# Optimization experiments

Hardware: AMD Instinct MI355X
Metric: run time of the kernel (lower is better)

## Reference

```python
import jax, jax.numpy as jnp
import numpy as np
import math

B_GRAPHS = 256
L_NODES = 64
N_NODES = B_GRAPHS * L_NODES
N_EDGES = N_NODES * 4
HEADS = 8
D_INNER = 512
N_DAGS = 1
DIAMETER = 64


def setup_inputs() -> dict:
    key = jax.random.key(0)
    ks = jax.random.split(key, 8)
    x = jax.random.normal(ks[0], (N_NODES, D_INNER), jnp.float32)
    B = jax.random.normal(ks[1], (N_NODES, D_INNER), jnp.float32)
    C = jax.random.normal(ks[2], (N_NODES, D_INNER), jnp.float32)
    dt = jax.random.normal(ks[3], (N_NODES, N_DAGS * HEADS * 2), jnp.float32)
    dt_edge = jax.random.normal(ks[4], (N_EDGES, N_DAGS * HEADS), jnp.float32)
    # DAG edges: within each graph, src_local < dst_local (gap 1..7) -> strictly upper triangular
    u = jax.random.randint(ks[5], (N_EDGES,), 0, L_NODES - 1)
    gap = jax.random.randint(ks[6], (N_EDGES,), 1, 8)
    v = jnp.minimum(u + gap, L_NODES - 1)
    graph = jnp.arange(N_EDGES) // (N_EDGES // B_GRAPHS)
    edge_index = jnp.stack([graph * L_NODES + u, graph * L_NODES + v]).astype(jnp.int32)
    data_batch = (jnp.arange(N_NODES) // L_NODES).astype(jnp.int32)
    dag_masks = jnp.ones((N_DAGS, N_EDGES), jnp.float32)
    # dt_bias init as in module __init__ (inverse softplus of dt in [1e-3, 1e-1])
    rng = np.random.default_rng(0)
    dtv = np.exp(rng.uniform(size=(HEADS,)) * (math.log(0.1) - math.log(0.001)) + math.log(0.001))
    dtv = np.clip(dtv, 1e-4, None)
    dt_bias = jnp.asarray(dtv + np.log(-np.expm1(-dtv)), jnp.float32)
    D = jnp.ones((HEADS,), jnp.float32)
    return dict(x=x, B=B, C=C, dt=dt, dt_edge=dt_edge, dt_bias=dt_bias, D=D,
                dag_masks=dag_masks, edge_index=edge_index, data_batch=data_batch,
                diameter=DIAMETER)


def _repeated_squaring_inverse(A, diam):
    # (I - A)^{-1} = prod_k (I + A^{2^k}) for nilpotent A; O(log diam) matmuls
    j = 2 ** int(math.ceil(math.log2(diam)))
    I = jnp.eye(A.shape[-1], dtype=A.dtype)
    last = A
    M = I + A
    for _ in range(2, int(math.log2(j)) + 1):
        last = last @ last
        M = M @ (I + last)
    return M


def reference(x, B, C, dt, dt_edge, dt_bias, D, dag_masks, edge_index, data_batch, diameter):
    N, din = x.shape
    g, E = dag_masks.shape
    n = dt_bias.shape[0]
    b = int(data_batch[-1]) + 1
    l = N // b  # equal-size graphs -> dense batching is a reshape, mask all-True
    h = din // n
    src, dst = edge_index[0], edge_index[1]

    # dt_node: (N, g*n*c) -> (c, g, n, N); softplus(dt + bias)
    c = dt.shape[1] // (g * n)
    dtn = dt.reshape(N, g, n, c).transpose(3, 1, 2, 0)
    dtn = jax.nn.softplus(dtn + dt_bias[None, None, :, None])
    dte = dt_edge.reshape(E, g, n).transpose(1, 2, 0)  # (g,n,E)
    dte = jax.nn.softplus(dte + dt_bias[None, :, None])

    dt_s, dt_t = dtn[0], dtn[1]
    dt_sum = (dt_s[:, :, src] + dt_t[:, :, dst] + dte) / np.sqrt(3.0)  # (g,n,E)
    dt_exp = jnp.exp(-dt_sum)
    msk = dag_masks[:, None, :]
    dt_sum = dt_sum * msk
    dt_exp = dt_exp * msk

    # dense adjacency with per-edge attrs; note 'b l1 l2 (g n) -> b g n l2 l1' transpose
    b_e = src // l
    sl = src % l
    dl = dst % l
    attr = dt_exp.transpose(2, 0, 1).reshape(E, g * n)
    adj = jnp.zeros((b, l, l, g * n), x.dtype).at[b_e, sl, dl].add(attr)
    A = adj.reshape(b, l, l, g, n).transpose(0, 3, 4, 2, 1)  # (b,g,n,l,l)

    # normalize_mat: sqrt outer product of in-degree counts, clamped at 1
    ec = jnp.zeros((g, N), x.dtype).at[:, dst].add(dag_masks)
    ec_dense = ec.T.reshape(b, l, g)
    outer = jnp.sqrt(jnp.einsum('blg,btg->bglt', ec_dense, ec_dense))
    outer = jnp.where(outer < 1.0, 1.0, outer)
    A = A / outer[:, :, None]

    dnorm = jnp.zeros((g, n, N), x.dtype).at[:, :, dst].add(dt_sum)
    dnorm = dnorm.transpose(2, 0, 1).reshape(b, l, g, n).transpose(0, 2, 3, 1)  # (b,g,n,l)

    A2 = A.reshape(b, g * n, l, l).astype(jnp.float32)
    L = _repeated_squaring_inverse(A2, int(diameter))
    L = L.reshape(b, g, n, l, l) * dnorm[..., None]

    x4 = x.reshape(b, l, n, h).transpose(0, 2, 1, 3)  # (b,n,l,h)
    B3 = B.reshape(b, l, -1)
    C3 = C.reshape(b, l, -1)
    # y = einsum(C,L,B,x) with B/C broadcast over (g,n): fold C.B^T into L
    CB = jnp.einsum('bld,btd->blt', C3, B3)
    M = L * CB[:, None, None]
    y = jnp.einsum('bgnlt,bnth->bgnlh', M, x4)
    y = y + x4[:, None] * D[None, None, :, None, None]
    y = y.transpose(0, 3, 1, 2, 4).reshape(N, g, n * h)  # b g n l h -> (N, g, n*h)
    y = y.sum(axis=1) / np.sqrt(g)
    return y
```

## Files before the change

### kernel.cpp

```cpp
#include <hip/hip_runtime.h>
#include <math.h>

#define NGRAPH 256
#define HEADS  8
#define DIN    512
#define EPG    256
#define NEDGE  65536
#define LOG2E 1.44269504088896341f
#define LN2   0.69314718055994531f

typedef short bf16x8 __attribute__((ext_vector_type(8)));
typedef float f32x4 __attribute__((ext_vector_type(4)));
typedef unsigned long long u64;

__device__ __forceinline__ float softplusf(float v) {
    if (v > 20.f) return v;
    float t = exp2f(v * LOG2E);
    return LN2 * log2f(1.f + t);
}
__device__ __forceinline__ unsigned short f2bf(float f) {
    union { float f; unsigned u; } c; c.f = f;
    unsigned r = c.u + 0x7fffu + ((c.u >> 16) & 1u);
    return (unsigned short)(r >> 16);
}
__device__ __forceinline__ float bf2f(unsigned short h) {
    union { float f; unsigned u; } c; c.u = ((unsigned)h) << 16;
    return c.f;
}
__device__ __forceinline__ int swz_idx(int row, int t) {
    int g = ((t >> 3) ^ (row ^ (row >> 3))) & 7;
    return (row << 6) | (g << 3) | (t & 7);
}
__device__ __forceinline__ void split1(float f, unsigned short& hi, unsigned short& lo) {
    union { float f; unsigned q; } c; c.f = f;
    unsigned hb = c.q & 0xffff0000u;
    hi = (unsigned short)(hb >> 16);
    union { float f; unsigned q; } d; d.q = hb;
    union { float f; unsigned q; } e2; e2.f = f - d.f;
    lo = (unsigned short)(e2.q >> 16);
}

__global__ __launch_bounds__(512, 2) void dag_pipe_v6(
        const float* __restrict__ x,
        const float* __restrict__ Bm,
        const float* __restrict__ Cm,
        const float* __restrict__ dt,
        const float* __restrict__ dt_edge,
        const float* __restrict__ dt_bias,
        const float* __restrict__ Dp,
        const float* __restrict__ dag_masks,
        const int* __restrict__ edge_index,
        float* __restrict__ out) {
    __shared__ __align__(16) unsigned short WS[32768];
    __shared__ __align__(16) unsigned short Xt[HEADS][4096];
    __shared__ __align__(16) unsigned short CBsh[4096];
    __shared__ __align__(16) float Ab8[HEADS][512];
    __shared__ float dts[HEADS][64];
    __shared__ float dtt[HEADS][64];
    __shared__ float ecsh[HEADS][64];

    const int b = blockIdx.x;
    const int tid = threadIdx.x;
    const int w = tid >> 6;
    const int lane = tid & 63;
    const int lm = lane & 15;
    const int quad = lane >> 4;
    const float bias = dt_bias[w];

    float2 dv = *(const float2*)(dt + ((size_t)(b * 64 + lane)) * 16 + w * 2);

    const int u0 = tid * 4;
    const int mat = u0 >> 10;
    const int srow = (u0 & 1023) >> 4;
    const int scol = (u0 & 15) << 2;
    const float* sp = (mat ? Bm : Cm) + ((size_t)(b * 64 + srow)) * DIN + scol;

    float4 pre0[4], pre1[4];
    #pragma unroll
    for (int i = 0; i < 4; ++i) pre0[i] = *(const float4*)(sp + 0 * 64 + 4 * i);
    #pragma unroll
    for (int i = 0; i < 4; ++i) pre1[i] = *(const float4*)(sp + 1 * 64 + 4 * i);

    int esl[4], edl[4]; float emk[4], edr[4];
    #pragma unroll
    for (int eo = 0; eo < 4; ++eo) {
        int e = b * EPG + eo * 64 + lane;
        esl[eo] = edge_index[e];
        edl[eo] = edge_index[NEDGE + e];
        emk[eo] = dag_masks[e];
        edr[eo] = dt_edge[(size_t)e * HEADS + w];
    }

    float4 xv[16];
    const float* xg = x + (size_t)b * 64 * DIN + w * 64;
    #pragma unroll
    for (int r = 0; r < 4; ++r) {
        int t0 = quad * 4 + r * 16;
        #pragma unroll
        for (int k = 0; k < 4; ++k)
            xv[r * 4 + k] = *(const float4*)(xg + (size_t)(t0 + k) * DIN + lm * 4);
    }

    dts[w][lane] = softplusf(dv.x + bias);
    dtt[w][lane] = softplusf(dv.y + bias);
    ecsh[w][lane] = 0.f;
    {
        float4 z = make_float4(0.f, 0.f, 0.f, 0.f);
        *(float4*)(&Ab8[w][lane * 8]) = z;
        *(float4*)(&Ab8[w][lane * 8 + 4]) = z;
    }

    #pragma unroll
    for (int eo = 0; eo < 4; ++eo) {
        int sl = esl[eo] & 63;
        int dl = edl[eo] & 63;
        float de = softplusf(edr[eo] + bias);
        float dsum = (dts[w][sl] + dtt[w][dl] + de) * 0.57735026918962576451f;
        float dexp = exp2f(-dsum * LOG2E);
        atomicAdd(&Ab8[w][dl * 8 + (dl - sl)], dexp * emk[eo]);
        atomicAdd(&Ab8[w][dl * 8], dsum * emk[eo]);
        atomicAdd(&ecsh[w][dl], emk[eo]);
    }

    const int mi = w >> 1;
    const int ni0 = (w & 1) * 2;
    f32x4 acc0 = {0.f, 0.f, 0.f, 0.f};
    f32x4 acc1 = {0.f, 0.f, 0.f, 0.f};
    #pragma unroll
    for (int c = 0; c < 8; ++c) {
        unsigned short* buf = WS + (c & 1) * 16384;
        unsigned short* thi = buf + mat * 8192;
        #pragma unroll
        for (int i = 0; i < 4; ++i) {
            float4 v = (c & 1) ? pre1[i] : pre0[i];
            float a[4] = {v.x, v.y, v.z, v.w};
            u64 hp = 0, lp = 0;
            #pragma unroll
            for (int k = 0; k < 4; ++k) {
                unsigned short h, l;
                split1(a[k], h, l);
                hp |= ((u64)h) << (16 * k);
                lp |= ((u64)l) << (16 * k);
            }
            int idx = swz_idx(srow, scol + 4 * i);
            *(u64*)(thi + idx) = hp;
            *(u64*)(thi + 4096 + idx) = lp;
        }
        if (c + 2 < 8) {
            #pragma unroll
            for (int i = 0; i < 4; ++i) {
                float4 nv = *(const float4*)(sp + (c + 2) * 64 + 4 * i);
                if (c & 1) pre1[i] = nv; else pre0[i] = nv;
            }
        }
        __syncthreads();
        const unsigned short* p = buf;
        #pragma unroll
        for (int ks = 0; ks < 2; ++ks) {
            int kl = ks * 32 + quad * 8;
            bf16x8 ah  = *(const bf16x8*)(p +         swz_idx(mi * 16 + lm, kl));
            bf16x8 al  = *(const bf16x8*)(p +  4096 + swz_idx(mi * 16 + lm, kl));
            bf16x8 b0h = *(const bf16x8*)(p +  8192 + swz_idx(ni0 * 16 + lm, kl));
            bf16x8 b0l = *(const bf16x8*)(p + 12288 + swz_idx(ni0 * 16 + lm, kl));
            bf16x8 b1h = *(const bf16x8*)(p +  8192 + swz_idx((ni0 + 1) * 16 + lm, kl));
            bf16x8 b1l = *(const bf16x8*)(p + 12288 + swz_idx((ni0 + 1) * 16 + lm, kl));
            acc0 = __builtin_amdgcn_mfma_f32_16x16x32_bf16(ah, b0h, acc0, 0, 0, 0);
            acc0 = __builtin_amdgcn_mfma_f32_16x16x32_bf16(ah, b0l, acc0, 0, 0, 0);
            acc0 = __builtin_amdgcn_mfma_f32_16x16x32_bf16(al, b0h, acc0, 0, 0, 0);
            acc1 = __builtin_amdgcn_mfma_f32_16x16x32_bf16(ah, b1h, acc1, 0, 0, 0);
            acc1 = __builtin_amdgcn_mfma_f32_16x16x32_bf16(ah, b1l, acc1, 0, 0, 0);
            acc1 = __builtin_amdgcn_mfma_f32_16x16x32_bf16(al, b1h, acc1, 0, 0, 0);
        }
    }
    #pragma unroll
    for (int r = 0; r < 4; ++r) {
        int row = mi * 16 + quad * 4 + r;
        CBsh[row * 64 + ni0 * 16 + lm] = f2bf(acc0[r]);
        CBsh[row * 64 + (ni0 + 1) * 16 + lm] = f2bf(acc1[r]);
    }

    {
        int e0 = lm * 4;
        #pragma unroll
        for (int r = 0; r < 4; ++r) {
            int t0 = quad * 4 + r * 16;
            float A0[4] = {xv[r*4+0].x, xv[r*4+0].y, xv[r*4+0].z, xv[r*4+0].w};
            float A1[4] = {xv[r*4+1].x, xv[r*4+1].y, xv[r*4+1].z, xv[r*4+1].w};
            float A2[4] = {xv[r*4+2].x, xv[r*4+2].y, xv[r*4+2].z, xv[r*4+2].w};
            float A3[4] = {xv[r*4+3].x, xv[r*4+3].y, xv[r*4+3].z, xv[r*4+3].w};
            #pragma unroll
            for (int k = 0; k < 4; ++k) {
                u64 pk = (u64)f2bf(A0[k])
                       | ((u64)f2bf(A1[k]) << 16)
                       | ((u64)f2bf(A2[k]) << 32)
                       | ((u64)f2bf(A3[k]) << 48);
                *(u64*)(&Xt[w][swz_idx(e0 + k, t0)]) = pk;
            }
        }
    }

    __syncthreads();

    {
        float eci = ecsh[w][lane];
        float4 a03 = *(const float4*)(&Ab8[w][lane * 8]);
        float4 a47 = *(const float4*)(&Ab8[w][lane * 8 + 4]);
        float sc[7];
        #pragma unroll
        for (int s = 0; s < 7; ++s) {
            int src = lane - 1 - s;
            float p = (src >= 0) ? eci * ecsh[w][src] : 1.f;
            sc[s] = fminf(1.f, rsqrtf(p));
        }
        a03.y *= sc[0]; a03.z *= sc[1]; a03.w *= sc[2];
        a47.x *= sc[3]; a47.y *= sc[4]; a47.z *= sc[5]; a47.w *= sc[6];
        *(float4*)(&Ab8[w][lane * 8]) = a03;
        *(float4*)(&Ab8[w][lane * 8 + 4]) = a47;
    }

    unsigned short* Wlw = WS + w * 4096;
    {
        const int j = lane;
        const float Dh = Dp[w];
        float mwin[7] = {0.f, 0.f, 0.f, 0.f, 0.f, 0.f, 0.f};
        float4 a03 = *(const float4*)(&Ab8[w][0]);
        float4 a47 = *(const float4*)(&Ab8[w][4]);
        float cbv = bf2f(CBsh[j]);
        #pragma unroll 2
        for (int i = 0; i < 64; ++i) {
            float4 n03, n47;
            float ncb = 0.f;
            if (i < 63) {
                n03 = *(const float4*)(&Ab8[w][(i + 1) * 8]);
                n47 = *(const float4*)(&Ab8[w][(i + 1) * 8 + 4]);
                ncb = bf2f(CBsh[(i + 1) * 64 + j]);
            } else {
                n03 = make_float4(0.f, 0.f, 0.f, 0.f);
                n47 = n03;
            }
            float diag = (j == i) ? 1.f : 0.f;
            float t0 = fmaf(a03.y, mwin[0], fmaf(a03.z, mwin[1], diag));
            float t1 = fmaf(a03.w, mwin[2], fmaf(a47.x, mwin[3], a47.y * mwin[4]));
            float t2 = fmaf(a47.z, mwin[5], a47.w * mwin[6]);
            float mi_ = t0 + (t1 + t2);
            float wv = mi_ * cbv * a03.x;
            if (j == i) wv += Dh;
            Wlw[swz_idx(i, j)] = f2bf(wv);
            #pragma unroll
            for (int s = 6; s > 0; --s) mwin[s] = mwin[s - 1];
            mwin[0] = mi_;
            a03 = n03; a47 = n47; cbv = ncb;
        }
    }

    {
        bf16x8 bfr[4][2];
        #pragma unroll
        for (int eb = 0; eb < 4; ++eb) {
            int er = eb * 16 + lm;
            bfr[eb][0] = *(const bf16x8*)(&Xt[w][swz_idx(er, quad * 8)]);
            bfr[eb][1] = *(const bf16x8*)(&Xt[w][swz_idx(er, 32 + quad * 8)]);
        }
        float* og = out + ((size_t)b * 64) * DIN + w * 64;
        #pragma unroll
        for (int m2 = 0; m2 < 4; ++m2) {
            int row0 = m2 * 16 + lm;
            bf16x8 a0 = *(const bf16x8*)(&Wlw[swz_idx(row0, quad * 8)]);
            bf16x8 a1 = *(const bf16x8*)(&Wlw[swz_idx(row0, 32 + quad * 8)]);
            f32x4 acc[4];
            #pragma unroll
            for (int eb = 0; eb < 4; ++eb) {
                f32x4 z = {0.f, 0.f, 0.f, 0.f};
                z = __builtin_amdgcn_mfma_f32_16x16x32_bf16(a0, bfr[eb][0], z, 0, 0, 0);
                z = __builtin_amdgcn_mfma_f32_16x16x32_bf16(a1, bfr[eb][1], z, 0, 0, 0);
                acc[eb] = z;
            }
            #pragma unroll
            for (int r = 0; r < 4; ++r) {
                int row = m2 * 16 + quad * 4 + r;
                #pragma unroll
                for (int eb = 0; eb < 4; ++eb)
                    og[(size_t)row * DIN + eb * 16 + lm] = acc[eb][r];
            }
        }
    }
}

extern "C" void kernel_launch(void* const* d_in, const int* in_sizes, int n_in,
                              void* d_out, int out_size, void* d_ws, size_t ws_size,
                              hipStream_t stream) {
    (void)in_sizes; (void)n_in; (void)out_size; (void)d_ws; (void)ws_size;
    dag_pipe_v6<<<dim3(NGRAPH), dim3(512), 0, stream>>>(
        (const float*)d_in[0],
        (const float*)d_in[1],
        (const float*)d_in[2],
        (const float*)d_in[3],
        (const float*)d_in[4],
        (const float*)d_in[5],
        (const float*)d_in[6],
        (const float*)d_in[7],
        (const int*)d_in[8],
        (float*)d_out);
}
```

Baseline: 163.6 us.

## Compute CB with single-pass bf16 MFMA and interleave edge scatter into K loop

New measurement: 161.3 us. No clear change (-1.4%).

```diff
diff --git a/kernel.cpp b/kernel.cpp
--- a/kernel.cpp
+++ b/kernel.cpp
@@ -27,20 +27,21 @@
     union { float f; unsigned u; } c; c.u = ((unsigned)h) << 16;
     return c.f;
 }
+__device__ __forceinline__ u64 pack4(float4 v) {
+    return (u64)f2bf(v.x) | ((u64)f2bf(v.y) << 16)
+         | ((u64)f2bf(v.z) << 32) | ((u64)f2bf(v.w) << 48);
+}
 __device__ __forceinline__ int swz_idx(int row, int t) {
     int g = ((t >> 3) ^ (row ^ (row >> 3))) & 7;
     return (row << 6) | (g << 3) | (t & 7);
 }
-__device__ __forceinline__ void split1(float f, unsigned short& hi, unsigned short& lo) {
-    union { float f; unsigned q; } c; c.f = f;
-    unsigned hb = c.q & 0xffff0000u;
-    hi = (unsigned short)(hb >> 16);
-    union { float f; unsigned q; } d; d.q = hb;
-    union { float f; unsigned q; } e2; e2.f = f - d.f;
-    lo = (unsigned short)(e2.q >> 16);
-}
-
-__global__ __launch_bounds__(512, 2) void dag_pipe_v6(
+__device__ __forceinline__ int swz128(int row, int col) {
+    int g = col >> 3;
+    int gs = (g & 8) | ((g ^ row) & 7);
+    return row * 128 + (gs << 3) + (col & 7);
+}
+
+__global__ __launch_bounds__(512, 2) void dag_v7(
         const float* __restrict__ x,
         const float* __restrict__ Bm,
         const float* __restrict__ Cm,
@@ -69,18 +70,6 @@
 
     float2 dv = *(const float2*)(dt + ((size_t)(b * 64 + lane)) * 16 + w * 2);
 
-    const int u0 = tid * 4;
-    const int mat = u0 >> 10;
-    const int srow = (u0 & 1023) >> 4;
-    const int scol = (u0 & 15) << 2;
-    const float* sp = (mat ? Bm : Cm) + ((size_t)(b * 64 + srow)) * DIN + scol;
-
-    float4 pre0[4], pre1[4];
-    #pragma unroll
-    for (int i = 0; i < 4; ++i) pre0[i] = *(const float4*)(sp + 0 * 64 + 4 * i);
-    #pragma unroll
-    for (int i = 0; i < 4; ++i) pre1[i] = *(const float4*)(sp + 1 * 64 + 4 * i);
-
     int esl[4], edl[4]; float emk[4], edr[4];
     #pragma unroll
     for (int eo = 0; eo < 4; ++eo) {
@@ -91,14 +80,15 @@
         edr[eo] = dt_edge[(size_t)e * HEADS + w];
     }
 
-    float4 xv[16];
-    const float* xg = x + (size_t)b * 64 * DIN + w * 64;
-    #pragma unroll
-    for (int r = 0; r < 4; ++r) {
-        int t0 = quad * 4 + r * 16;
-        #pragma unroll
-        for (int k = 0; k < 4; ++k)
-            xv[r * 4 + k] = *(const float4*)(xg + (size_t)(t0 + k) * DIN + lm * 4);
+    const int srow = tid >> 3;
+    const int scol = (tid & 7) << 4;
+    const float* Cp = Cm + ((size_t)(b * 64 + srow)) * DIN + scol;
+    const float* Bp = Bm + ((size_t)(b * 64 + srow)) * DIN + scol;
+    float4 pre[8];
+    #pragma unroll
+    for (int i = 0; i < 4; ++i) {
+        pre[i]     = *(const float4*)(Cp + 4 * i);
+        pre[4 + i] = *(const float4*)(Bp + 4 * i);
     }
 
     dts[w][lane] = softplusf(dv.x + bias);
@@ -108,68 +98,57 @@
         float4 z = make_float4(0.f, 0.f, 0.f, 0.f);
         *(float4*)(&Ab8[w][lane * 8]) = z;
         *(float4*)(&Ab8[w][lane * 8 + 4]) = z;
-    }
-
-    #pragma unroll
-    for (int eo = 0; eo < 4; ++eo) {
-        int sl = esl[eo] & 63;
-        int dl = edl[eo] & 63;
-        float de = softplusf(edr[eo] + bias);
-        float dsum = (dts[w][sl] + dtt[w][dl] + de) * 0.57735026918962576451f;
-        float dexp = exp2f(-dsum * LOG2E);
-        atomicAdd(&Ab8[w][dl * 8 + (dl - sl)], dexp * emk[eo]);
-        atomicAdd(&Ab8[w][dl * 8], dsum * emk[eo]);
-        atomicAdd(&ecsh[w][dl], emk[eo]);
     }
 
     const int mi = w >> 1;
     const int ni0 = (w & 1) * 2;
     f32x4 acc0 = {0.f, 0.f, 0.f, 0.f};
     f32x4 acc1 = {0.f, 0.f, 0.f, 0.f};
-    #pragma unroll
-    for (int c = 0; c < 8; ++c) {
+    float4 xv[16];
+    #pragma unroll
+    for (int c = 0; c < 4; ++c) {
         unsigned short* buf = WS + (c & 1) * 16384;
-        unsigned short* thi = buf + mat * 8192;
         #pragma unroll
         for (int i = 0; i < 4; ++i) {
-            float4 v = (c & 1) ? pre1[i] : pre0[i];
-            float a[4] = {v.x, v.y, v.z, v.w};
-            u64 hp = 0, lp = 0;
-            #pragma unroll
-            for (int k = 0; k < 4; ++k) {
-                unsigned short h, l;
-                split1(a[k], h, l);
-                hp |= ((u64)h) << (16 * k);
-                lp |= ((u64)l) << (16 * k);
-            }
-            int idx = swz_idx(srow, scol + 4 * i);
-            *(u64*)(thi + idx) = hp;
-            *(u64*)(thi + 4096 + idx) = lp;
-        }
-        if (c + 2 < 8) {
+            int col = scol + 4 * i;
+            *(u64*)(buf + swz128(srow, col))        = pack4(pre[i]);
+            *(u64*)(buf + 8192 + swz128(srow, col)) = pack4(pre[4 + i]);
+        }
+        if (c < 3) {
             #pragma unroll
             for (int i = 0; i < 4; ++i) {
-                float4 nv = *(const float4*)(sp + (c + 2) * 64 + 4 * i);
-                if (c & 1) pre1[i] = nv; else pre0[i] = nv;
+                pre[i]     = *(const float4*)(Cp + (c + 1) * 128 + 4 * i);
+                pre[4 + i] = *(const float4*)(Bp + (c + 1) * 128 + 4 * i);
+            }
+        } else {
+            const float* xg = x + (size_t)b * 64 * DIN + w * 64;
+            #pragma unroll
+            for (int r = 0; r < 4; ++r) {
+                int t0 = quad * 4 + r * 16;
+                #pragma unroll
+                for (int k = 0; k < 4; ++k)
+                    xv[r * 4 + k] = *(const float4*)(xg + (size_t)(t0 + k) * DIN + lm * 4);
             }
         }
         __syncthreads();
-        const unsigned short* p = buf;
-        #pragma unroll
-        for (int ks = 0; ks < 2; ++ks) {
+        #pragma unroll
+        for (int ks = 0; ks < 4; ++ks) {
             int kl = ks * 32 + quad * 8;
-            bf16x8 ah  = *(const bf16x8*)(p +         swz_idx(mi * 16 + lm, kl));
-            bf16x8 al  = *(const bf16x8*)(p +  4096 + swz_idx(mi * 16 + lm, kl));
-            bf16x8 b0h = *(const bf16x8*)(p +  8192 + swz_idx(ni0 * 16 + lm, kl));
-            bf16x8 b0l = *(const bf16x8*)(p + 12288 + swz_idx(ni0 * 16 + lm, kl));
-            bf16x8 b1h = *(const bf16x8*)(p +  8192 + swz_idx((ni0 + 1) * 16 + lm, kl));
-            bf16x8 b1l = *(const bf16x8*)(p + 12288 + swz_idx((ni0 + 1) * 16 + lm, kl));
-            acc0 = __builtin_amdgcn_mfma_f32_16x16x32_bf16(ah, b0h, acc0, 0, 0, 0);
-            acc0 = __builtin_amdgcn_mfma_f32_16x16x32_bf16(ah, b0l, acc0, 0, 0, 0);
-            acc0 = __builtin_amdgcn_mfma_f32_16x16x32_bf16(al, b0h, acc0, 0, 0, 0);
-            acc1 = __builtin_amdgcn_mfma_f32_16x16x32_bf16(ah, b1h, acc1, 0, 0, 0);
-            acc1 = __builtin_amdgcn_mfma_f32_16x16x32_bf16(ah, b1l, acc1, 0, 0, 0);
-            acc1 = __builtin_amdgcn_mfma_f32_16x16x32_bf16(al, b1h, acc1, 0, 0, 0);
+            bf16x8 ah = *(const bf16x8*)(buf + swz128(mi * 16 + lm, kl));
+            bf16x8 b0 = *(const bf16x8*)(buf + 8192 + swz128(ni0 * 16 + lm, kl));
+            bf16x8 b1 = *(const bf16x8*)(buf + 8192 + swz128((ni0 + 1) * 16 + lm, kl));
+            acc0 = __builtin_amdgcn_mfma_f32_16x16x32_bf16(ah, b0, acc0, 0, 0, 0);
+            acc1 = __builtin_amdgcn_mfma_f32_16x16x32_bf16(ah, b1, acc1, 0, 0, 0);
+        }
+        {
+            int sl = esl[c] & 63;
+            int dl = edl[c] & 63;
+            float de = softplusf(edr[c] + bias);
+            float dsum = (dts[w][sl] + dtt[w][dl] + de) * 0.57735026918962576451f;
+            float dexp = exp2f(-dsum * LOG2E);
+            atomicAdd(&Ab8[w][dl * 8 + (dl - sl)], dexp * emk[c]);
+            atomicAdd(&Ab8[w][dl * 8], dsum * emk[c]);
+            atomicAdd(&ecsh[w][dl], emk[c]);
         }
     }
     #pragma unroll
@@ -216,6 +195,14 @@
         a47.x *= sc[3]; a47.y *= sc[4]; a47.z *= sc[5]; a47.w *= sc[6];
         *(float4*)(&Ab8[w][lane * 8]) = a03;
         *(float4*)(&Ab8[w][lane * 8 + 4]) = a47;
+    }
+
+    bf16x8 bfr[4][2];
+    #pragma unroll
+    for (int eb = 0; eb < 4; ++eb) {
+        int er = eb * 16 + lm;
+        bfr[eb][0] = *(const bf16x8*)(&Xt[w][swz_idx(er, quad * 8)]);
+        bfr[eb][1] = *(const bf16x8*)(&Xt[w][swz_idx(er, 32 + quad * 8)]);
     }
 
     unsigned short* Wlw = WS + w * 4096;
@@ -254,13 +241,6 @@
     }
 
     {
-        bf16x8 bfr[4][2];
-        #pragma unroll
-        for (int eb = 0; eb < 4; ++eb) {
-            int er = eb * 16 + lm;
-            bfr[eb][0] = *(const bf16x8*)(&Xt[w][swz_idx(er, quad * 8)]);
-            bfr[eb][1] = *(const bf16x8*)(&Xt[w][swz_idx(er, 32 + quad * 8)]);
-        }
         float* og = out + ((size_t)b * 64) * DIN + w * 64;
         #pragma unroll
         for (int m2 = 0; m2 < 4; ++m2) {
@@ -290,7 +270,7 @@
                               void* d_out, int out_size, void* d_ws, size_t ws_size,
                               hipStream_t stream) {
     (void)in_sizes; (void)n_in; (void)out_size; (void)d_ws; (void)ws_size;
-    dag_pipe_v6<<<dim3(NGRAPH), dim3(512), 0, stream>>>(
+    dag_v7<<<dim3(NGRAPH), dim3(512), 0, stream>>>(
         (const float*)d_in[0],
         (const float*)d_in[1],
         (const float*)d_in[2],
```
